# Optimization experiments

Measured on AMD Instinct MI355X. Metric: run time of the kernel, lower is better.

## Reference

```python
import jax, jax.numpy as jnp
import numpy as np

HIDDEN = 4096
N_HEADS = 32
N_KV_HEADS = 8
HEAD_DIM = HIDDEN // N_HEADS  # 128
Q_SIZE = N_HEADS * HEAD_DIM
KV_SIZE = N_KV_HEADS * HEAD_DIM
ROPE_THETA = 10000.0
EPS = 1e-5
SCALE = HEAD_DIM ** -0.5


def _headwise_layernorm(x, weight, eps):
    # x: [B,S,H,D], weight: [H,D]; LayerNorm over last dim (head_dim), fp32 math
    xf = x.astype(jnp.float32)
    mean = xf.mean(-1, keepdims=True)
    var = jnp.square(xf - mean).mean(-1, keepdims=True)
    y = (xf - mean) * jax.lax.rsqrt(var + eps)
    return (weight.astype(jnp.float32) * y).astype(x.dtype)


def _rope_gptj(x, positions):
    # non-neox (GPT-J) style: rotate interleaved pairs. x: [B,S,H,D]
    half = HEAD_DIM // 2
    inv_freq = 1.0 / (ROPE_THETA ** (jnp.arange(0, HEAD_DIM, 2, dtype=jnp.float32) / HEAD_DIM))
    ang = positions.astype(jnp.float32)[..., None] * inv_freq  # [B,S,half]
    cos = jnp.cos(ang)[:, :, None, :]  # [B,S,1,half]
    sin = jnp.sin(ang)[:, :, None, :]
    x1 = x[..., 0::2]
    x2 = x[..., 1::2]
    o1 = x1 * cos - x2 * sin
    o2 = x2 * cos + x1 * sin
    # re-interleave
    out = jnp.stack([o1, o2], axis=-1).reshape(x.shape)
    return out.astype(x.dtype)


def setup_inputs() -> dict:
    key = jax.random.key(0)
    k1, k2, k3, k4 = jax.random.split(key, 4)
    B, S = 2, 2048
    positions = jnp.tile(jnp.arange(S, dtype=jnp.int32)[None, :], (B, 1))
    hidden_states = jax.random.normal(k1, (B, S, HIDDEN), dtype=jnp.float32)
    Wqkv = jax.random.normal(k2, (HIDDEN, Q_SIZE + 2 * KV_SIZE), dtype=jnp.float32) * (HIDDEN ** -0.5)
    Wo = jax.random.normal(k3, (Q_SIZE, HIDDEN), dtype=jnp.float32) * (Q_SIZE ** -0.5)
    kq, kk = jax.random.split(k4)
    q_norm_w = jnp.ones((N_HEADS, HEAD_DIM), jnp.float32) + 0.02 * jax.random.normal(kq, (N_HEADS, HEAD_DIM))
    k_norm_w = jnp.ones((N_KV_HEADS, HEAD_DIM), jnp.float32) + 0.02 * jax.random.normal(kk, (N_KV_HEADS, HEAD_DIM))
    return {"positions": positions, "hidden_states": hidden_states, "Wqkv": Wqkv,
            "q_norm_w": q_norm_w, "k_norm_w": k_norm_w, "Wo": Wo}


def reference(positions, hidden_states, Wqkv, q_norm_w, k_norm_w, Wo):
    B, S, _ = hidden_states.shape
    qkv = hidden_states @ Wqkv  # [B,S,Q+2KV]
    q, k, v = jnp.split(qkv, [Q_SIZE, Q_SIZE + KV_SIZE], axis=-1)
    q = q.reshape(B, S, N_HEADS, HEAD_DIM)
    k = k.reshape(B, S, N_KV_HEADS, HEAD_DIM)
    v = v.reshape(B, S, N_KV_HEADS, HEAD_DIM)
    # per-head qk-norm
    q = _headwise_layernorm(q, q_norm_w, EPS)
    k = _headwise_layernorm(k, k_norm_w, EPS)
    # non-neox RoPE
    q = _rope_gptj(q, positions)
    k = _rope_gptj(k, positions)
    # GQA: repeat kv heads
    n_rep = N_HEADS // N_KV_HEADS
    k = jnp.repeat(k, n_rep, axis=2)  # [B,S,H,D]
    v = jnp.repeat(v, n_rep, axis=2)
    scores = jnp.einsum('bqhd,bkhd->bhqk', q, k) * SCALE
    causal = jnp.tril(jnp.ones((S, S), dtype=bool))
    scores = jnp.where(causal[None, None], scores, jnp.finfo(scores.dtype).min)
    probs = jax.nn.softmax(scores, axis=-1)
    attn = jnp.einsum('bhqk,bkhd->bqhd', probs, v).reshape(B, S, Q_SIZE)
    return attn @ Wo
```

## Files before the change

kernel.cpp:

```cpp
#include <hip/hip_runtime.h>
#include <hip/hip_bf16.h>
#include <cstdint>

typedef unsigned short u16;
typedef unsigned int u32;
typedef __attribute__((ext_vector_type(8))) short bf16x8;
typedef __attribute__((ext_vector_type(4))) float f32x4;
typedef __attribute__((ext_vector_type(16))) float f32x16;
typedef __attribute__((ext_vector_type(4))) unsigned int u32x4;

#define HIDDEN 4096
#define NH 32
#define NKV 8
#define HD 128
#define QSZ 4096
#define KVSZ 1024
#define QKV_N 6144
#define SEQ 2048
#define NB 2
#define NTOK (NB*SEQ)
#define ATT_SCALE 0.08838834764831845f
#define LOG2E 1.4426950408889634f
#define LN_EPS 1e-5f
#define THRD 12.0f

__device__ __forceinline__ u16 f2bf(float f) {
  union { float f; u32 u; } a; a.f = f;
  u32 r = a.u + 0x7fffu + ((a.u >> 16) & 1u);
  return (u16)(r >> 16);
}
__device__ __forceinline__ float bf2f(u16 h) {
  union { u32 u; float f; } a; a.u = ((u32)h) << 16;
  return a.f;
}

__device__ __forceinline__ void gload_lds16(const void* g, void* l) {
  __builtin_amdgcn_global_load_lds(
      (const __attribute__((address_space(1))) void*)g,
      (__attribute__((address_space(3))) void*)l,
      16, 0, 0);
}

__global__ __launch_bounds__(256)
void conv_f32_bf16(const float* __restrict__ in, u16* __restrict__ out, int n8) {
  int i = blockIdx.x * 256 + threadIdx.x;
  if (i >= n8) return;
  const float4* p = (const float4*)in + (size_t)i * 2;
  float4 v0 = p[0], v1 = p[1];
  u32x4 o;
  o.x = (u32)f2bf(v0.x) | ((u32)f2bf(v0.y) << 16);
  o.y = (u32)f2bf(v0.z) | ((u32)f2bf(v0.w) << 16);
  o.z = (u32)f2bf(v1.x) | ((u32)f2bf(v1.y) << 16);
  o.w = (u32)f2bf(v1.z) | ((u32)f2bf(v1.w) << 16);
  ((u32x4*)out)[i] = o;
}

__global__ __launch_bounds__(256)
void transp_f32_bf16(const float* __restrict__ in, u16* __restrict__ out, int R, int C) {
  __shared__ float tile[32][33];
  int c0 = blockIdx.x << 5, r0 = blockIdx.y << 5;
  int tx = threadIdx.x & 31, ty = threadIdx.x >> 5;
  #pragma unroll
  for (int j = 0; j < 32; j += 8)
    tile[ty + j][tx] = in[(long)(r0 + ty + j) * C + c0 + tx];
  __syncthreads();
  #pragma unroll
  for (int j = 0; j < 32; j += 8)
    out[(long)(c0 + ty + j) * R + r0 + tx] = f2bf(tile[tx][ty + j]);
}

template<typename OutT>
__global__ __launch_bounds__(512, 2)
void gemm_bt2(const u16* __restrict__ A, const u16* __restrict__ Bt,
              OutT* __restrict__ C, int N, int K) {
  extern __shared__ char smem[];
  const int t = threadIdx.x;
  const int lane = t & 63, w = t >> 6;
  const int wr = w >> 2, wc = w & 3;
  const int l31 = lane & 31, l7 = lane & 7, g2 = lane >> 5;

  const int nbn = N >> 8;
  const int cpx = gridDim.x >> 3;
  const int wg = (blockIdx.x & 7) * cpx + (blockIdx.x >> 3);
  const int bm = wg / nbn, bn = wg - bm * nbn;

  const int ciA0 = t, ciA1 = t + 512;
  const u16* AgS0 = A + (long)(bm * 128 + (ciA0 >> 3)) * K + (((ciA0 & 7) ^ ((ciA0 >> 3) & 7)) << 3);
  const u16* AgS1 = A + (long)(bm * 128 + (ciA1 >> 3)) * K + (((ciA1 & 7) ^ ((ciA1 >> 3) & 7)) << 3);
  const u16* BgS0;
  const u16* BgS1;
  const u16* BgS2;
  const u16* BgS3;
  {
    int ci0 = t, ci1 = t + 512, ci2 = t + 1024, ci3 = t + 1536;
    BgS0 = Bt + (long)(bn * 256 + (ci0 >> 3)) * K + (((ci0 & 7) ^ ((ci0 >> 3) & 7)) << 3);
    BgS1 = Bt + (long)(bn * 256 + (ci1 >> 3)) * K + (((ci1 & 7) ^ ((ci1 >> 3) & 7)) << 3);
    BgS2 = Bt + (long)(bn * 256 + (ci2 >> 3)) * K + (((ci2 & 7) ^ ((ci2 >> 3) & 7)) << 3);
    BgS3 = Bt + (long)(bn * 256 + (ci3 >> 3)) * K + (((ci3 & 7) ^ ((ci3 >> 3) & 7)) << 3);
  }
  const int dA0 = (w * 64) * 16;
  const int dA1 = (512 + w * 64) * 16;
  const int dB0 = 16384 + (w * 64) * 16;
  const int dB1 = 16384 + (512 + w * 64) * 16;
  const int dB2 = 16384 + (1024 + w * 64) * 16;
  const int dB3 = 16384 + (1536 + w * 64) * 16;

  const int arow0 = (wr * 64 + l31) * 128;
  const int brow0 = 16384 + (wc * 64 + l31) * 128;

  f32x16 acc[2][2];
  #pragma unroll
  for (int i = 0; i < 2; ++i)
    #pragma unroll
    for (int j = 0; j < 2; ++j)
      #pragma unroll
      for (int r = 0; r < 16; ++r) acc[i][j][r] = 0.f;

  const int nt = K >> 6;
  char* cbase = smem;
  char* nbase = smem + 49152;
  char* sbase = smem + 98304;

  gload_lds16(AgS0, cbase + dA0);  gload_lds16(AgS1, cbase + dA1);
  gload_lds16(BgS0, cbase + dB0);  gload_lds16(BgS1, cbase + dB1);
  gload_lds16(BgS2, cbase + dB2);  gload_lds16(BgS3, cbase + dB3);
  gload_lds16(AgS0 + 64, nbase + dA0);  gload_lds16(AgS1 + 64, nbase + dA1);
  gload_lds16(BgS0 + 64, nbase + dB0);  gload_lds16(BgS1 + 64, nbase + dB1);
  gload_lds16(BgS2 + 64, nbase + dB2);  gload_lds16(BgS3 + 64, nbase + dB3);
  asm volatile("s_waitcnt vmcnt(6)" ::: "memory");
  __builtin_amdgcn_s_barrier();
  __builtin_amdgcn_sched_barrier(0);

  for (int tt = 0; tt < nt; ++tt) {
    const long sk = (long)((tt + 2 < nt) ? (tt + 2) : (nt - 1)) * 64;
    bf16x8 aF[2][2], bF[2][2];
    #pragma unroll
    for (int kk = 0; kk < 2; ++kk) {
      const int pcb = ((kk * 2 + g2) ^ l7) * 16;
      #pragma unroll
      for (int mf = 0; mf < 2; ++mf)
        aF[kk][mf] = *(const bf16x8*)(cbase + arow0 + mf * 32 * 128 + pcb);
      #pragma unroll
      for (int nf = 0; nf < 2; ++nf)
        bF[kk][nf] = *(const bf16x8*)(cbase + brow0 + nf * 32 * 128 + pcb);
    }
    gload_lds16(AgS0 + sk, sbase + dA0);
    gload_lds16(AgS1 + sk, sbase + dA1);
    __builtin_amdgcn_s_barrier();
    __builtin_amdgcn_sched_barrier(0);
    __builtin_amdgcn_s_setprio(1);
    #pragma unroll
    for (int kk = 0; kk < 2; ++kk)
      #pragma unroll
      for (int mf = 0; mf < 2; ++mf)
        #pragma unroll
        for (int nf = 0; nf < 2; ++nf)
          acc[mf][nf] = __builtin_amdgcn_mfma_f32_32x32x16_bf16(aF[kk][mf], bF[kk][nf], acc[mf][nf], 0, 0, 0);
    __builtin_amdgcn_s_setprio(0);
    __builtin_amdgcn_sched_barrier(0);
    __builtin_amdgcn_s_barrier();
    __builtin_amdgcn_sched_barrier(0);
    #pragma unroll
    for (int kk = 0; kk < 2; ++kk) {
      const int pcb = (((kk + 2) * 2 + g2) ^ l7) * 16;
      #pragma unroll
      for (int mf = 0; mf < 2; ++mf)
        aF[kk][mf] = *(const bf16x8*)(cbase + arow0 + mf * 32 * 128 + pcb);
      #pragma unroll
      for (int nf = 0; nf < 2; ++nf)
        bF[kk][nf] = *(const bf16x8*)(cbase + brow0 + nf * 32 * 128 + pcb);
    }
    gload_lds16(BgS0 + sk, sbase + dB0);
    gload_lds16(BgS1 + sk, sbase + dB1);
    gload_lds16(BgS2 + sk, sbase + dB2);
    gload_lds16(BgS3 + sk, sbase + dB3);
    asm volatile("s_waitcnt vmcnt(6)" ::: "memory");
    __builtin_amdgcn_s_barrier();
    __builtin_amdgcn_sched_barrier(0);
    __builtin_amdgcn_s_setprio(1);
    #pragma unroll
    for (int kk = 0; kk < 2; ++kk)
      #pragma unroll
      for (int mf = 0; mf < 2; ++mf)
        #pragma unroll
        for (int nf = 0; nf < 2; ++nf)
          acc[mf][nf] = __builtin_amdgcn_mfma_f32_32x32x16_bf16(aF[kk][mf], bF[kk][nf], acc[mf][nf], 0, 0, 0);
    __builtin_amdgcn_s_setprio(0);
    __builtin_amdgcn_sched_barrier(0);
    __builtin_amdgcn_s_barrier();
    __builtin_amdgcn_sched_barrier(0);
    char* tmp = cbase; cbase = nbase; nbase = sbase; sbase = tmp;
  }

  #pragma unroll
  for (int mf = 0; mf < 2; ++mf)
    #pragma unroll
    for (int nf = 0; nf < 2; ++nf)
      #pragma unroll
      for (int r = 0; r < 16; ++r) {
        long row = bm * 128 + wr * 64 + mf * 32 + (r & 3) + 8 * (r >> 2) + 4 * g2;
        long col = bn * 256 + wc * 64 + nf * 32 + l31;
        float v = acc[mf][nf][r];
        if constexpr (sizeof(OutT) == 2) C[row * N + col] = f2bf(v);
        else                             C[row * N + col] = v;
      }
}

__device__ __forceinline__ void ln_rope_head(const u16* __restrict__ src,
                                             const float* __restrict__ wgt,
                                             u16* __restrict__ dst,
                                             int lane, float sa, float ca, float scale) {
  u32 xr = *(const u32*)(src + 2 * lane);
  float x1 = bf2f((u16)(xr & 0xffffu)), x2 = bf2f((u16)(xr >> 16));
  float ssum = x1 + x2;
  #pragma unroll
  for (int off = 1; off < 64; off <<= 1) ssum += __shfl_xor(ssum, off);
  float mean = ssum * (1.0f / 128.0f);
  float e1 = x1 - mean, e2 = x2 - mean;
  float vv = e1 * e1 + e2 * e2;
  #pragma unroll
  for (int off = 1; off < 64; off <<= 1) vv += __shfl_xor(vv, off);
  float rstd = rsqrtf(vv * (1.0f / 128.0f) + LN_EPS);
  float y1 = e1 * rstd * wgt[2 * lane];
  float y2 = e2 * rstd * wgt[2 * lane + 1];
  float o1 = (y1 * ca - y2 * sa) * scale;
  float o2 = (y2 * ca + y1 * sa) * scale;
  *(u32*)(dst + 2 * lane) = (u32)f2bf(o1) | ((u32)f2bf(o2) << 16);
}

__global__ __launch_bounds__(512)
void ln_rope(const u16* __restrict__ qkv, const int* __restrict__ pos,
             const float* __restrict__ qw, const float* __restrict__ kw,
             u16* __restrict__ qo, u16* __restrict__ ko) {
  const int s = blockIdx.x, b = blockIdx.y;
  const int t = threadIdx.x, lane = t & 63, w = t >> 6;
  const long base = (long)(b * SEQ + s) * QKV_N;
  const int p = pos[b * SEQ + s];
  const float expo = (float)(2 * lane) * (1.0f / 128.0f);
  const float inv_freq = exp2f(-expo * 13.287712379549449f);
  float sa, ca;
  sincosf((float)p * inv_freq, &sa, &ca);
  #pragma unroll
  for (int hh = 0; hh < 4; ++hh) {
    int h = w + hh * 8;
    ln_rope_head(qkv + base + h * HD, qw + h * HD,
                 qo + (((long)b * NH + h) * SEQ + s) * HD, lane, sa, ca,
                 ATT_SCALE * LOG2E);
  }
  ln_rope_head(qkv + base + QSZ + w * HD, kw + w * HD,
               ko + (((long)b * NKV + w) * SEQ + s) * HD, lane, sa, ca, 1.0f);
}

__global__ __launch_bounds__(256)
void v_transp(const u16* __restrict__ qkv, u16* __restrict__ vt) {
  __shared__ u16 tile[32][33];
  int s0 = blockIdx.x * 32, d0 = blockIdx.y * 32;
  int bk = blockIdx.z;
  int b = bk >> 3, kvh = bk & 7;
  int tx = threadIdx.x & 31, ty = threadIdx.x >> 5;
  const u16* src = qkv + ((long)(b * SEQ) + s0) * QKV_N + QSZ + KVSZ + kvh * HD + d0;
  #pragma unroll
  for (int j = 0; j < 32; j += 8)
    tile[ty + j][tx] = src[(long)(ty + j) * QKV_N + tx];
  __syncthreads();
  u16* dst = vt + (((long)bk) * HD + d0) * SEQ + s0;
  #pragma unroll
  for (int j = 0; j < 32; j += 8)
    dst[(long)(ty + j) * SEQ + tx] = tile[tx][ty + j];
}

__global__ __launch_bounds__(512, 2)
void flash_attn2(const u16* __restrict__ Qg, const u16* __restrict__ Kg,
                 const u16* __restrict__ Vtg, u16* __restrict__ Og) {
  const int lin = blockIdx.x;
  const int b = lin >> 8;
  const int rem = lin & 255;
  const int h = rem >> 3;
  const int q3 = rem & 7;
  const int qt = b ? (7 - q3) : q3;
  const int kvh = h >> 2;
  const int t = threadIdx.x, lane = t & 63, w = t >> 6;
  const int hh = lane >> 5, l31 = lane & 31;
  const int wq0 = qt * 256 + w * 32;
  const int q = wq0 + l31;

  __shared__ u16 Klds[2][64 * 128];
  __shared__ u16 Vlds[2][128 * 64];

  const u16* Qbase = Qg + (((long)b * NH + h) * SEQ + q) * HD + hh * 8;
  bf16x8 qf[8];
  #pragma unroll
  for (int ks = 0; ks < 8; ++ks) qf[ks] = *(const bf16x8*)(Qbase + ks * 16);

  f32x16 o[4];
  #pragma unroll
  for (int i = 0; i < 4; ++i)
    #pragma unroll
    for (int r = 0; r < 16; ++r) o[i][r] = 0.f;
  float m = -1e30f, l = 0.f;

  const u16* Kbase = Kg + ((long)b * NKV + kvh) * (long)SEQ * HD;
  const u16* Vtbase = Vtg + ((long)b * NKV + kvh) * (long)HD * SEQ;
  const int nt = qt * 4 + 4;

  auto STAGE = [&](int buf, int kt) {
    const int kv0 = kt * 64;
    #pragma unroll
    for (int i = 0; i < 2; ++i) {
      int c = t + i * 512;
      int kv = c >> 4, cc = c & 15;
      int cl = (cc & 8) | ((cc ^ kv) & 7);
      gload_lds16(Kbase + (long)(kv0 + kv) * HD + cl * 8,
                  (char*)(&Klds[buf][0]) + (i * 512 + w * 64) * 16);
    }
    #pragma unroll
    for (int i = 0; i < 2; ++i) {
      int c = t + i * 512;
      int d = c >> 3, cc = c & 7;
      int cl = cc ^ (d & 7);
      gload_lds16(Vtbase + (long)d * SEQ + kv0 + cl * 8,
                  (char*)(&Vlds[buf][0]) + (i * 512 + w * 64) * 16);
    }
  };

  STAGE(0, 0);
  __syncthreads();
  int cur = 0;
  for (int kt = 0; kt < nt; ++kt) {
    const int kv0 = kt * 64;
    if (kt + 1 < nt) STAGE(cur ^ 1, kt + 1);
    if (kv0 <= wq0 + 31) {
      const char* Kb = (const char*)(&Klds[cur][0]);
      const char* Vb = (const char*)(&Vlds[cur][0]);
      f32x16 st[2];
      #pragma unroll
      for (int tt = 0; tt < 2; ++tt)
        #pragma unroll
        for (int r = 0; r < 16; ++r) st[tt][r] = 0.f;
      __builtin_amdgcn_s_setprio(1);
      #pragma unroll
      for (int tt = 0; tt < 2; ++tt) {
        if (kv0 + tt * 32 <= wq0 + 31) {
          #pragma unroll
          for (int ks = 0; ks < 8; ++ks) {
            int ch = ks * 2 + hh;
            int pc = (ch & 8) | ((ch ^ l31) & 7);
            bf16x8 kf = *(const bf16x8*)(Kb + (tt * 32 + l31) * 256 + pc * 16);
            st[tt] = __builtin_amdgcn_mfma_f32_32x32x16_bf16(kf, qf[ks], st[tt], 0, 0, 0);
          }
        }
      }
      __builtin_amdgcn_s_setprio(0);
      if (kv0 + 63 > wq0) {
        #pragma unroll
        for (int tt = 0; tt < 2; ++tt)
          #pragma unroll
          for (int r = 0; r < 16; ++r) {
            int kva = kv0 + tt * 32 + (r & 3) + 8 * (r >> 2) + 4 * hh;
            if (kva > q) st[tt][r] = -1e30f;
          }
      }
      float p0 = -1e30f, p1 = -1e30f, p2 = -1e30f, p3 = -1e30f;
      #pragma unroll
      for (int tt = 0; tt < 2; ++tt)
        #pragma unroll
        for (int r = 0; r < 16; r += 4) {
          p0 = fmaxf(p0, st[tt][r]);
          p1 = fmaxf(p1, st[tt][r + 1]);
          p2 = fmaxf(p2, st[tt][r + 2]);
          p3 = fmaxf(p3, st[tt][r + 3]);
        }
      float mx = fmaxf(fmaxf(p0, p1), fmaxf(p2, p3));
      mx = fmaxf(mx, __shfl_xor(mx, 32));
      if (!__all(mx - m <= THRD)) {
        float mn = fmaxf(m, mx);
        float sc = exp2f(m - mn);
        m = mn;
        float scr[16];
        #pragma unroll
        for (int r = 0; r < 16; ++r)
          scr[r] = __shfl(sc, (r & 3) + 8 * (r >> 2) + 4 * hh);
        #pragma unroll
        for (int db = 0; db < 4; ++db)
          #pragma unroll
          for (int r = 0; r < 16; ++r) o[db][r] *= scr[r];
        l *= sc;
      }
      float s0 = 0.f, s1 = 0.f, s2 = 0.f, s3 = 0.f;
      #pragma unroll
      for (int tt = 0; tt < 2; ++tt)
        #pragma unroll
        for (int r = 0; r < 16; r += 4) {
          float e0 = exp2f(st[tt][r] - m);
          float e1 = exp2f(st[tt][r + 1] - m);
          float e2 = exp2f(st[tt][r + 2] - m);
          float e3 = exp2f(st[tt][r + 3] - m);
          st[tt][r] = e0; st[tt][r + 1] = e1; st[tt][r + 2] = e2; st[tt][r + 3] = e3;
          s0 += e0; s1 += e1; s2 += e2; s3 += e3;
        }
      float rs = (s0 + s1) + (s2 + s3);
      rs += __shfl_xor(rs, 32);
      l += rs;
      bf16x8 pa[4];
      #pragma unroll
      for (int k4 = 0; k4 < 4; ++k4) {
        int s8 = (k4 & 1) * 8, tt = k4 >> 1;
        u32 x0 = (u32)f2bf(st[tt][s8 + 0]) | ((u32)f2bf(st[tt][s8 + 1]) << 16);
        u32 x1 = (u32)f2bf(st[tt][s8 + 2]) | ((u32)f2bf(st[tt][s8 + 3]) << 16);
        u32 y0 = (u32)f2bf(st[tt][s8 + 4]) | ((u32)f2bf(st[tt][s8 + 5]) << 16);
        u32 y1 = (u32)f2bf(st[tt][s8 + 6]) | ((u32)f2bf(st[tt][s8 + 7]) << 16);
        u32 x0s = (u32)__shfl_xor((int)x0, 32), x1s = (u32)__shfl_xor((int)x1, 32);
        u32 y0s = (u32)__shfl_xor((int)y0, 32), y1s = (u32)__shfl_xor((int)y1, 32);
        union { u32 u[4]; bf16x8 v; } pk;
        pk.u[0] = hh ? y0s : x0;
        pk.u[1] = hh ? y1s : x1;
        pk.u[2] = hh ? y0 : x0s;
        pk.u[3] = hh ? y1 : x1s;
        pa[k4] = pk.v;
      }
      __builtin_amdgcn_s_setprio(1);
      #pragma unroll
      for (int k4 = 0; k4 < 4; ++k4)
        #pragma unroll
        for (int db = 0; db < 4; ++db) {
          int ch = k4 * 2 + hh;
          int pcc = ch ^ (l31 & 7);
          bf16x8 vf = *(const bf16x8*)(Vb + (db * 32 + l31) * 128 + pcc * 16);
          o[db] = __builtin_amdgcn_mfma_f32_32x32x16_bf16(pa[k4], vf, o[db], 0, 0, 0);
        }
      __builtin_amdgcn_s_setprio(0);
    }
    __syncthreads();
    cur ^= 1;
  }
  float linv = 1.0f / l;
  float li[16];
  #pragma unroll
  for (int r = 0; r < 16; ++r)
    li[r] = __shfl(linv, (r & 3) + 8 * (r >> 2) + 4 * hh);
  #pragma unroll
  for (int db = 0; db < 4; ++db)
    #pragma unroll
    for (int r = 0; r < 16; ++r) {
      int qr = wq0 + (r & 3) + 8 * (r >> 2) + 4 * hh;
      Og[((long)b * SEQ + qr) * QSZ + h * HD + db * 32 + l31] = f2bf(o[db][r] * li[r]);
    }
}

extern "C" void kernel_launch(void* const* d_in, const int* in_sizes, int n_in,
                              void* d_out, int out_size, void* d_ws, size_t ws_size,
                              hipStream_t stream) {
  const int*   positions = (const int*)d_in[0];
  const float* hidden    = (const float*)d_in[1];
  const float* Wqkv      = (const float*)d_in[2];
  const float* qnw       = (const float*)d_in[3];
  const float* knw       = (const float*)d_in[4];
  const float* Wo        = (const float*)d_in[5];
  float* out = (float*)d_out;
  char* ws = (char*)d_ws;
  const size_t MB = 1024 * 1024;
  u16* hbf   = (u16*)(ws + 0);
  u16* WqkvT = (u16*)(ws + 32 * MB);
  u16* qkvb  = (u16*)(ws + 80 * MB);
  u16* q_arr = (u16*)(ws + 0);
  u16* k_arr = (u16*)(ws + 32 * MB);
  u16* vt_arr= (u16*)(ws + 40 * MB);
  u16* WoT   = (u16*)(ws + 48 * MB);
  u16* Oarr  = (u16*)(ws + 80 * MB);

  const int GEMM_LDS = 3 * 49152;
  (void)hipFuncSetAttribute((const void*)&gemm_bt2<u16>,
        hipFuncAttributeMaxDynamicSharedMemorySize, GEMM_LDS);
  (void)hipFuncSetAttribute((const void*)&gemm_bt2<float>,
        hipFuncAttributeMaxDynamicSharedMemorySize, GEMM_LDS);

  conv_f32_bf16<<<dim3(NTOK * HIDDEN / 8 / 256), 256, 0, stream>>>(hidden, hbf, NTOK * HIDDEN / 8);
  transp_f32_bf16<<<dim3(QKV_N / 32, HIDDEN / 32), 256, 0, stream>>>(Wqkv, WqkvT, HIDDEN, QKV_N);
  gemm_bt2<u16><<<dim3((NTOK / 128) * (QKV_N / 256)), 512, GEMM_LDS, stream>>>(hbf, WqkvT, qkvb, QKV_N, HIDDEN);
  ln_rope<<<dim3(SEQ, NB), 512, 0, stream>>>(qkvb, positions, qnw, knw, q_arr, k_arr);
  v_transp<<<dim3(SEQ / 32, HD / 32, NB * NKV), 256, 0, stream>>>(qkvb, vt_arr);
  transp_f32_bf16<<<dim3(HIDDEN / 32, QSZ / 32), 256, 0, stream>>>(Wo, WoT, QSZ, HIDDEN);
  flash_attn2<<<dim3(512), 512, 0, stream>>>(q_arr, k_arr, vt_arr, Oarr);
  gemm_bt2<float><<<dim3((NTOK / 128) * (HIDDEN / 256)), 512, GEMM_LDS, stream>>>(Oarr, WoT, out, HIDDEN, QSZ);
}
```

Measured before the change: 618.7 us.

## Software-pipeline LDS reads with MFMA in GEMM and use plain 2D grid

The GEMM main loop is restructured so that fragment reads from LDS for the next k-slice are interleaved with MFMA on the current slice, and two intermediate barriers per iteration are removed. The XCD-aware block swizzle is replaced with a plain 2D grid mapping (bm = blockIdx.y, bn = blockIdx.x). The aim is to hide LDS latency and cut synchronisation stalls. Dropping the swizzle may hurt L2 locality across XCDs, and fewer barriers rely on the triple-buffer timing for correctness.

```diff
diff --git a/kernel.cpp b/kernel.cpp
--- a/kernel.cpp
+++ b/kernel.cpp
@@ -78,11 +78,7 @@
   const int lane = t & 63, w = t >> 6;
   const int wr = w >> 2, wc = w & 3;
   const int l31 = lane & 31, l7 = lane & 7, g2 = lane >> 5;
-
-  const int nbn = N >> 8;
-  const int cpx = gridDim.x >> 3;
-  const int wg = (blockIdx.x & 7) * cpx + (blockIdx.x >> 3);
-  const int bm = wg / nbn, bn = wg - bm * nbn;
+  const int bm = blockIdx.y, bn = blockIdx.x;
 
   const int ciA0 = t, ciA1 = t + 512;
   const u16* AgS0 = A + (long)(bm * 128 + (ciA0 >> 3)) * K + (((ciA0 & 7) ^ ((ciA0 >> 3) & 7)) << 3);
@@ -131,66 +127,44 @@
   __builtin_amdgcn_s_barrier();
   __builtin_amdgcn_sched_barrier(0);
 
+  #define READ_KK(dst, kkv) { \
+    const int pcb = (((kkv) * 2 + g2) ^ l7) * 16; \
+    dst[0] = *(const bf16x8*)(cbase + arow0 + pcb); \
+    dst[1] = *(const bf16x8*)(cbase + arow0 + 32 * 128 + pcb); \
+    dst[2] = *(const bf16x8*)(cbase + brow0 + pcb); \
+    dst[3] = *(const bf16x8*)(cbase + brow0 + 32 * 128 + pcb); }
+  #define MFMA_KK(src) { \
+    __builtin_amdgcn_s_setprio(1); \
+    acc[0][0] = __builtin_amdgcn_mfma_f32_32x32x16_bf16(src[0], src[2], acc[0][0], 0, 0, 0); \
+    acc[0][1] = __builtin_amdgcn_mfma_f32_32x32x16_bf16(src[0], src[3], acc[0][1], 0, 0, 0); \
+    acc[1][0] = __builtin_amdgcn_mfma_f32_32x32x16_bf16(src[1], src[2], acc[1][0], 0, 0, 0); \
+    acc[1][1] = __builtin_amdgcn_mfma_f32_32x32x16_bf16(src[1], src[3], acc[1][1], 0, 0, 0); \
+    __builtin_amdgcn_s_setprio(0); }
+
   for (int tt = 0; tt < nt; ++tt) {
     const long sk = (long)((tt + 2 < nt) ? (tt + 2) : (nt - 1)) * 64;
-    bf16x8 aF[2][2], bF[2][2];
-    #pragma unroll
-    for (int kk = 0; kk < 2; ++kk) {
-      const int pcb = ((kk * 2 + g2) ^ l7) * 16;
-      #pragma unroll
-      for (int mf = 0; mf < 2; ++mf)
-        aF[kk][mf] = *(const bf16x8*)(cbase + arow0 + mf * 32 * 128 + pcb);
-      #pragma unroll
-      for (int nf = 0; nf < 2; ++nf)
-        bF[kk][nf] = *(const bf16x8*)(cbase + brow0 + nf * 32 * 128 + pcb);
-    }
+    bf16x8 fA[4], fB[4];
+    READ_KK(fA, 0);
+    READ_KK(fB, 1);
     gload_lds16(AgS0 + sk, sbase + dA0);
     gload_lds16(AgS1 + sk, sbase + dA1);
-    __builtin_amdgcn_s_barrier();
-    __builtin_amdgcn_sched_barrier(0);
-    __builtin_amdgcn_s_setprio(1);
-    #pragma unroll
-    for (int kk = 0; kk < 2; ++kk)
-      #pragma unroll
-      for (int mf = 0; mf < 2; ++mf)
-        #pragma unroll
-        for (int nf = 0; nf < 2; ++nf)
-          acc[mf][nf] = __builtin_amdgcn_mfma_f32_32x32x16_bf16(aF[kk][mf], bF[kk][nf], acc[mf][nf], 0, 0, 0);
-    __builtin_amdgcn_s_setprio(0);
-    __builtin_amdgcn_sched_barrier(0);
-    __builtin_amdgcn_s_barrier();
-    __builtin_amdgcn_sched_barrier(0);
-    #pragma unroll
-    for (int kk = 0; kk < 2; ++kk) {
-      const int pcb = (((kk + 2) * 2 + g2) ^ l7) * 16;
-      #pragma unroll
-      for (int mf = 0; mf < 2; ++mf)
-        aF[kk][mf] = *(const bf16x8*)(cbase + arow0 + mf * 32 * 128 + pcb);
-      #pragma unroll
-      for (int nf = 0; nf < 2; ++nf)
-        bF[kk][nf] = *(const bf16x8*)(cbase + brow0 + nf * 32 * 128 + pcb);
-    }
+    MFMA_KK(fA);
+    READ_KK(fA, 2);
     gload_lds16(BgS0 + sk, sbase + dB0);
     gload_lds16(BgS1 + sk, sbase + dB1);
+    MFMA_KK(fB);
+    READ_KK(fB, 3);
     gload_lds16(BgS2 + sk, sbase + dB2);
     gload_lds16(BgS3 + sk, sbase + dB3);
+    MFMA_KK(fA);
+    MFMA_KK(fB);
     asm volatile("s_waitcnt vmcnt(6)" ::: "memory");
-    __builtin_amdgcn_s_barrier();
-    __builtin_amdgcn_sched_barrier(0);
-    __builtin_amdgcn_s_setprio(1);
-    #pragma unroll
-    for (int kk = 0; kk < 2; ++kk)
-      #pragma unroll
-      for (int mf = 0; mf < 2; ++mf)
-        #pragma unroll
-        for (int nf = 0; nf < 2; ++nf)
-          acc[mf][nf] = __builtin_amdgcn_mfma_f32_32x32x16_bf16(aF[kk][mf], bF[kk][nf], acc[mf][nf], 0, 0, 0);
-    __builtin_amdgcn_s_setprio(0);
-    __builtin_amdgcn_sched_barrier(0);
     __builtin_amdgcn_s_barrier();
     __builtin_amdgcn_sched_barrier(0);
     char* tmp = cbase; cbase = nbase; nbase = sbase; sbase = tmp;
   }
+  #undef READ_KK
+  #undef MFMA_KK
 
   #pragma unroll
   for (int mf = 0; mf < 2; ++mf)
@@ -476,10 +450,10 @@
 
   conv_f32_bf16<<<dim3(NTOK * HIDDEN / 8 / 256), 256, 0, stream>>>(hidden, hbf, NTOK * HIDDEN / 8);
   transp_f32_bf16<<<dim3(QKV_N / 32, HIDDEN / 32), 256, 0, stream>>>(Wqkv, WqkvT, HIDDEN, QKV_N);
-  gemm_bt2<u16><<<dim3((NTOK / 128) * (QKV_N / 256)), 512, GEMM_LDS, stream>>>(hbf, WqkvT, qkvb, QKV_N, HIDDEN);
+  gemm_bt2<u16><<<dim3(QKV_N / 256, NTOK / 128), 512, GEMM_LDS, stream>>>(hbf, WqkvT, qkvb, QKV_N, HIDDEN);
   ln_rope<<<dim3(SEQ, NB), 512, 0, stream>>>(qkvb, positions, qnw, knw, q_arr, k_arr);
   v_transp<<<dim3(SEQ / 32, HD / 32, NB * NKV), 256, 0, stream>>>(qkvb, vt_arr);
   transp_f32_bf16<<<dim3(HIDDEN / 32, QSZ / 32), 256, 0, stream>>>(Wo, WoT, QSZ, HIDDEN);
   flash_attn2<<<dim3(512), 512, 0, stream>>>(q_arr, k_arr, vt_arr, Oarr);
-  gemm_bt2<float><<<dim3((NTOK / 128) * (HIDDEN / 256)), 512, GEMM_LDS, stream>>>(Oarr, WoT, out, HIDDEN, QSZ);
-}
+  gemm_bt2<float><<<dim3(HIDDEN / 256, NTOK / 128), 512, GEMM_LDS, stream>>>(Oarr, WoT, out, HIDDEN, QSZ);
+}
```

Result: faster. 581.2 us (-6.1%).
